# Kernel optimization log

Hardware: AMD Instinct MI355X
Metric: run time of the kernel (lower is better)

The kernel has to match this reference:

```python
import jax, jax.numpy as jnp
import numpy as np

B, Q, K, H = 8, 2048, 2048, 512


def setup_inputs() -> dict:
    key = jax.random.key(0)
    ks = jax.random.split(key, 12)
    s = 1.0 / np.sqrt(H)
    return {
        "query": jax.random.normal(ks[0], (B, Q, H), jnp.float32),
        "key_": jax.random.normal(ks[1], (B, K, H), jnp.float32),
        "value": jax.random.normal(ks[2], (B, K, H), jnp.float32),
        "mask": jax.random.randint(ks[3], (B, K), 0, 2).astype(bool),
        "Wq": jax.random.normal(ks[4], (H, H), jnp.float32) * s,
        "bq": jnp.zeros((H,), jnp.float32),
        "Wk": jax.random.normal(ks[5], (H, H), jnp.float32) * s,
        "bk": jnp.zeros((H,), jnp.float32),
        "Wv": jax.random.normal(ks[6], (H, H), jnp.float32) * s,
        "bv": jnp.zeros((H,), jnp.float32),
        "Wo": jax.random.normal(ks[7], (H, H), jnp.float32) * s,
        "bo": jnp.zeros((H,), jnp.float32),
    }


def reference(query, key_, value, mask, Wq, bq, Wk, bk, Wv, bv, Wo, bo):
    scale = jnp.sqrt(jnp.float32(H))
    Qp = query @ Wq + bq          # (B,Q,H)
    Kp = key_ @ Wk + bk           # (B,K,H)
    Vp = value @ Wv + bv          # (B,K,H)
    energy = jnp.einsum("bqh,bkh->bqk", Qp, Kp) / scale
    # mask is (B, key_len); torch code broadcasts it over all query rows
    energy = jnp.where(mask[:, None, :], -jnp.inf, energy)
    idx = jnp.argmax(energy, axis=-1)                 # (B,Q)
    score = jax.nn.one_hot(idx, K, dtype=energy.dtype)  # hardmax one-hot (B,Q,K)
    # score @ V is exactly a per-row gather of the argmax-selected V row
    res = jnp.take_along_axis(Vp, idx[:, :, None], axis=1)  # (B,Q,H)
    res = res @ Wo + bo
    return (res, score)
```

## Files before the change

kernel.cpp:

```cpp
#include <hip/hip_runtime.h>

typedef _Float16 f16;
typedef f16 f16x8 __attribute__((ext_vector_type(8)));
typedef f16 f16x4 __attribute__((ext_vector_type(4)));
typedef short s16x8 __attribute__((ext_vector_type(8)));
typedef short s16x4 __attribute__((ext_vector_type(4)));
typedef float f32x4 __attribute__((ext_vector_type(4)));

#define MFMA16(a,b,c)  __builtin_amdgcn_mfma_f32_16x16x32_f16(a,b,c,0,0,0)
#define MFMAB16(a,b,c) __builtin_amdgcn_mfma_f32_16x16x32_bf16(a,b,c,0,0,0)

static constexpr int Bn = 8, Qn = 2048, Kn = 2048, Hn = 512;
static constexpr int Mn = Bn * Qn;

typedef __attribute__((address_space(1))) const unsigned int as1_uint;
typedef __attribute__((address_space(3))) unsigned int as3_uint;

__device__ __forceinline__ void gl_lds16(const void* g, void* l) {
    __builtin_amdgcn_global_load_lds((as1_uint*)g, (as3_uint*)l, 16, 0, 0);
}

__device__ __forceinline__ short bf16r(float x) {
    unsigned u = __builtin_bit_cast(unsigned, x);
    u += 0x7fffu + ((u >> 16) & 1u);
    return (short)(u >> 16);
}

__device__ __forceinline__ int swz(int row) { return (row >> 1) & 3; }

__global__ __launch_bounds__(256) void prep_all(
    const int* __restrict__ mask, const float* __restrict__ Wk,
    const float* __restrict__ Wo, const float* __restrict__ bq,
    const float* __restrict__ bv, const float* __restrict__ bo,
    int* __restrict__ cidx, int* __restrict__ cnt,
    f16* __restrict__ Wk_h, f16* __restrict__ Wk_l, short* __restrict__ Wot,
    float* __restrict__ wvec, float* __restrict__ cvec)
{
    const int bid = blockIdx.x, t = threadIdx.x;
    if (bid < 8) {
        __shared__ int sums[256];
        int b = bid;
        int base = b * Kn + t * 8;
        int mv[8]; int s = 0;
        #pragma unroll
        for (int i = 0; i < 8; ++i) { mv[i] = (mask[base + i] == 0); s += mv[i]; }
        sums[t] = s;
        __syncthreads();
        for (int off = 1; off < 256; off <<= 1) {
            int v = (t >= off) ? sums[t - off] : 0;
            __syncthreads();
            sums[t] += v;
            __syncthreads();
        }
        int pos = (t > 0 ? sums[t - 1] : 0);
        #pragma unroll
        for (int i = 0; i < 8; ++i)
            if (mv[i]) cidx[b * Kn + pos++] = t * 8 + i;
        if (t == 255) {
            int total = sums[255];
            if (total == 0) { cidx[b * Kn] = 0; total = 1; }
            cnt[b] = total;
        }
    } else if (bid < 1032) {
        int e = (bid - 8) * 256 + t;
        float v = Wk[e] * 512.0f;
        f16 h = (f16)v;
        Wk_h[e] = h; Wk_l[e] = (f16)((v - (float)h) * 2048.0f);
        int r = e >> 9, c = e & 511;
        Wot[c * 512 + r] = bf16r(Wo[e]);
    } else {
        #pragma unroll
        for (int i = 0; i < 2; ++i) {
            int tt = t + i * 256;
            float s = 0.f;
            for (int n = 0; n < 512; n += 4) {
                f32x4 a = *(const f32x4*)(Wk + (size_t)tt * 512 + n);
                f32x4 q = *(const f32x4*)(bq + n);
                s += a[0]*q[0] + a[1]*q[1] + a[2]*q[2] + a[3]*q[3];
            }
            wvec[tt] = s * (1.0f / 512.0f);
            float s2 = 0.f;
            for (int h = 0; h < 512; ++h) s2 += bv[h] * Wo[h * 512 + tt];
            cvec[tt] = s2 + bo[tt];
        }
    }
}

template<int PREP>
__global__ __launch_bounds__(256) void gemm_split(
    const float* __restrict__ Af,
    const f16* __restrict__ Bh_g, const f16* __restrict__ Bl_g,
    f16* __restrict__ Oh, f16* __restrict__ Ol)
{
    __shared__ __align__(16) f16 Ah[2][2048], Al[2][2048], Bh[2][4096], Bl[2][4096];
    const int tid = threadIdx.x, lane = tid & 63, wid = tid >> 6;
    const int l15 = lane & 15, lg = lane >> 4;
    const int m0 = blockIdx.x * 64, n0 = blockIdx.y * 128;
    const int srow = lane >> 2, sg = lane & 3;
    const int ar0 = tid >> 3, ac0 = (tid & 7) * 4;

    auto stageB = [&](int buf, int ks) {
        const int k0 = ks << 5;
        #pragma unroll
        for (int h = 0; h < 2; ++h) {
            int s = wid + h * 4;
            int row = s * 16 + srow;
            int goff = k0 + ((sg ^ swz(row)) << 3);
            gl_lds16(Bh_g + (size_t)(n0 + row) * Hn + goff, &Bh[buf][s * 512]);
            gl_lds16(Bl_g + (size_t)(n0 + row) * Hn + goff, &Bl[buf][s * 512]);
        }
    };
    auto writeA = [&](int buf, const f32x4* av) {
        #pragma unroll
        for (int rr = 0; rr < 2; ++rr) {
            int row = ar0 + rr * 32;
            f16x4 oh, ol;
            #pragma unroll
            for (int j = 0; j < 4; ++j) {
                f16 hh = (f16)av[rr][j];
                oh[j] = hh;
                ol[j] = (f16)((av[rr][j] - (float)hh) * 2048.0f);
            }
            int off = row * 32 + (((ac0 >> 3) ^ swz(row)) << 3) + (ac0 & 7);
            *(f16x4*)&Ah[buf][off] = oh;
            *(f16x4*)&Al[buf][off] = ol;
        }
    };

    const float* aSrc[2];
    #pragma unroll
    for (int rr = 0; rr < 2; ++rr)
        aSrc[rr] = Af + (size_t)(m0 + ar0 + rr * 32) * Hn;

    f32x4 a0[4][2] = {}, a1[4][2] = {};
    {
        f32x4 av[2];
        #pragma unroll
        for (int rr = 0; rr < 2; ++rr) av[rr] = *(const f32x4*)(aSrc[rr] + ac0);
        stageB(0, 0);
        writeA(0, av);
    }
    __syncthreads();
    #pragma unroll 1
    for (int ks = 0; ks < 16; ++ks) {
        const int cur = ks & 1, nxt = cur ^ 1;
        f32x4 av[2];
        if (ks < 15) {
            const int k1 = (ks + 1) << 5;
            #pragma unroll
            for (int rr = 0; rr < 2; ++rr) av[rr] = *(const f32x4*)(aSrc[rr] + k1 + ac0);
            stageB(nxt, ks + 1);
        }
        f16x8 fbh[2], fbl[2];
        #pragma unroll
        for (int fj = 0; fj < 2; ++fj) {
            int row = wid * 32 + fj * 16 + l15;
            int off = row * 32 + ((lg ^ swz(row)) << 3);
            fbh[fj] = *(f16x8*)&Bh[cur][off];
            fbl[fj] = *(f16x8*)&Bl[cur][off];
        }
        #pragma unroll
        for (int fi = 0; fi < 4; ++fi) {
            int row = fi * 16 + l15;
            int off = row * 32 + ((lg ^ swz(row)) << 3);
            f16x8 fah = *(f16x8*)&Ah[cur][off];
            f16x8 fal = *(f16x8*)&Al[cur][off];
            #pragma unroll
            for (int fj = 0; fj < 2; ++fj) {
                a0[fi][fj] = MFMA16(fah, fbh[fj], a0[fi][fj]);
                a1[fi][fj] = MFMA16(fah, fbl[fj], a1[fi][fj]);
                a1[fi][fj] = MFMA16(fal, fbh[fj], a1[fi][fj]);
            }
        }
        if (ks < 15) writeA(nxt, av);
        __syncthreads();
    }
    #pragma unroll
    for (int fi = 0; fi < 4; ++fi)
    #pragma unroll
    for (int fj = 0; fj < 2; ++fj)
    #pragma unroll
    for (int j = 0; j < 4; ++j) {
        int m = m0 + fi * 16 + lg * 4 + j;
        int n = n0 + wid * 32 + fj * 16 + l15;
        float v = a0[fi][fj][j] + a1[fi][fj][j] * (1.0f / 2048.0f);
        if (PREP == 0) v *= (1.0f / 512.0f);
        f16 h = (f16)v;
        f16 lo = (f16)((v - (float)h) * 2048.0f);
        size_t o = PREP ? ((size_t)n * Hn + m) : ((size_t)m * Hn + n);
        Oh[o] = h; Ol[o] = lo;
    }
}

__global__ __launch_bounds__(256) void gemm_bfk0(
    const float* __restrict__ Af, const short* __restrict__ Bt,
    short* __restrict__ Out)
{
    __shared__ __align__(16) short As[2][2048], Bs[2][4096];
    const int tid = threadIdx.x, lane = tid & 63, wid = tid >> 6;
    const int l15 = lane & 15, lg = lane >> 4;
    const int m0 = blockIdx.x * 64, n0 = blockIdx.y * 128;
    const int srow = lane >> 2, sg = lane & 3;
    const int ar0 = tid >> 3, ac0 = (tid & 7) * 4;

    const float* aSrc[2];
    #pragma unroll
    for (int rr = 0; rr < 2; ++rr)
        aSrc[rr] = Af + (size_t)(m0 + ar0 + rr * 32) * Hn;

    auto stageB = [&](int buf, int ks) {
        const int k0 = ks << 5;
        #pragma unroll
        for (int h = 0; h < 2; ++h) {
            int s = wid + h * 4;
            int row = s * 16 + srow;
            int goff = k0 + ((sg ^ swz(row)) << 3);
            gl_lds16(Bt + (size_t)(n0 + row) * Hn + goff, &Bs[buf][s * 512]);
        }
    };
    auto writeA = [&](int buf, const f32x4* av) {
        #pragma unroll
        for (int rr = 0; rr < 2; ++rr) {
            int row = ar0 + rr * 32;
            s16x4 o;
            #pragma unroll
            for (int j = 0; j < 4; ++j) o[j] = bf16r(av[rr][j]);
            int off = row * 32 + (((ac0 >> 3) ^ swz(row)) << 3) + (ac0 & 7);
            *(s16x4*)&As[buf][off] = o;
        }
    };

    f32x4 acc[4][2] = {};
    {
        f32x4 av[2];
        #pragma unroll
        for (int rr = 0; rr < 2; ++rr) av[rr] = *(const f32x4*)(aSrc[rr] + ac0);
        stageB(0, 0);
        writeA(0, av);
    }
    __syncthreads();
    #pragma unroll 1
    for (int ks = 0; ks < 16; ++ks) {
        const int cur = ks & 1, nxt = cur ^ 1;
        f32x4 av[2];
        if (ks < 15) {
            const int k1 = (ks + 1) << 5;
            #pragma unroll
            for (int rr = 0; rr < 2; ++rr) av[rr] = *(const f32x4*)(aSrc[rr] + k1 + ac0);
            stageB(nxt, ks + 1);
        }
        s16x8 fb[2];
        #pragma unroll
        for (int fj = 0; fj < 2; ++fj) {
            int row = wid * 32 + fj * 16 + l15;
            fb[fj] = *(s16x8*)&Bs[cur][row * 32 + ((lg ^ swz(row)) << 3)];
        }
        #pragma unroll
        for (int fi = 0; fi < 4; ++fi) {
            int row = fi * 16 + l15;
            s16x8 fa = *(s16x8*)&As[cur][row * 32 + ((lg ^ swz(row)) << 3)];
            #pragma unroll
            for (int fj = 0; fj < 2; ++fj)
                acc[fi][fj] = MFMAB16(fa, fb[fj], acc[fi][fj]);
        }
        if (ks < 15) writeA(nxt, av);
        __syncthreads();
    }
    #pragma unroll
    for (int fi = 0; fi < 4; ++fi)
    #pragma unroll
    for (int fj = 0; fj < 2; ++fj)
    #pragma unroll
    for (int j = 0; j < 4; ++j) {
        int m = m0 + fi * 16 + lg * 4 + j;
        int n = n0 + wid * 32 + fj * 16 + l15;
        Out[(size_t)n * Hn + m] = bf16r(acc[fi][fj][j]);
    }
}

__global__ __launch_bounds__(256) void qm_kconv(
    const float* __restrict__ query,
    const f16* __restrict__ Mt_h, const f16* __restrict__ Mt_l,
    f16* __restrict__ qM_h, f16* __restrict__ qM_l,
    const float* __restrict__ key_, const int* __restrict__ cidx,
    const int* __restrict__ cnt, const float* __restrict__ wvec,
    f16* __restrict__ Kc_h, float* __restrict__ beta)
{
    __shared__ __align__(16) f16 smem[2][2048 + 2048 + 4096 + 4096];
    const int bid = blockIdx.x;
    const int tid = threadIdx.x, lane = tid & 63, wid = tid >> 6;
    if (bid < 1024) {
        f16 (*Ah)[2048+2048+4096+4096] = smem;
        #define AH(b,i) Ah[b][i]
        #define AL(b,i) Ah[b][2048 + (i)]
        #define BH(b,i) Ah[b][4096 + (i)]
        #define BL(b,i) Ah[b][8192 + (i)]
        const int l15 = lane & 15, lg = lane >> 4;
        const int m0 = (bid & 255) * 64, n0 = (bid >> 8) * 128;
        const int srow = lane >> 2, sg = lane & 3;
        const int ar0 = tid >> 3, ac0 = (tid & 7) * 4;

        auto stageB = [&](int buf, int ks) {
            const int k0 = ks << 5;
            #pragma unroll
            for (int h = 0; h < 2; ++h) {
                int s = wid + h * 4;
                int row = s * 16 + srow;
                int goff = k0 + ((sg ^ swz(row)) << 3);
                gl_lds16(Mt_h + (size_t)(n0 + row) * Hn + goff, &BH(buf, s * 512));
                gl_lds16(Mt_l + (size_t)(n0 + row) * Hn + goff, &BL(buf, s * 512));
            }
        };
        auto writeA = [&](int buf, const f32x4* av) {
            #pragma unroll
            for (int rr = 0; rr < 2; ++rr) {
                int row = ar0 + rr * 32;
                f16x4 oh, ol;
                #pragma unroll
                for (int j = 0; j < 4; ++j) {
                    f16 hh = (f16)av[rr][j];
                    oh[j] = hh;
                    ol[j] = (f16)((av[rr][j] - (float)hh) * 2048.0f);
                }
                int off = row * 32 + (((ac0 >> 3) ^ swz(row)) << 3) + (ac0 & 7);
                *(f16x4*)&AH(buf, off) = oh;
                *(f16x4*)&AL(buf, off) = ol;
            }
        };

        const float* aSrc[2];
        #pragma unroll
        for (int rr = 0; rr < 2; ++rr)
            aSrc[rr] = query + (size_t)(m0 + ar0 + rr * 32) * Hn;

        f32x4 a0[4][2] = {}, a1[4][2] = {};
        {
            f32x4 av[2];
            #pragma unroll
            for (int rr = 0; rr < 2; ++rr) av[rr] = *(const f32x4*)(aSrc[rr] + ac0);
            stageB(0, 0);
            writeA(0, av);
        }
        __syncthreads();
        #pragma unroll 1
        for (int ks = 0; ks < 16; ++ks) {
            const int cur = ks & 1, nxt = cur ^ 1;
            f32x4 av[2];
            if (ks < 15) {
                const int k1 = (ks + 1) << 5;
                #pragma unroll
                for (int rr = 0; rr < 2; ++rr) av[rr] = *(const f32x4*)(aSrc[rr] + k1 + ac0);
                stageB(nxt, ks + 1);
            }
            f16x8 fbh[2], fbl[2];
            #pragma unroll
            for (int fj = 0; fj < 2; ++fj) {
                int row = wid * 32 + fj * 16 + l15;
                int off = row * 32 + ((lg ^ swz(row)) << 3);
                fbh[fj] = *(f16x8*)&BH(cur, off);
                fbl[fj] = *(f16x8*)&BL(cur, off);
            }
            #pragma unroll
            for (int fi = 0; fi < 4; ++fi) {
                int row = fi * 16 + l15;
                int off = row * 32 + ((lg ^ swz(row)) << 3);
                f16x8 fah = *(f16x8*)&AH(cur, off);
                f16x8 fal = *(f16x8*)&AL(cur, off);
                #pragma unroll
                for (int fj = 0; fj < 2; ++fj) {
                    a0[fi][fj] = MFMA16(fah, fbh[fj], a0[fi][fj]);
                    a1[fi][fj] = MFMA16(fah, fbl[fj], a1[fi][fj]);
                    a1[fi][fj] = MFMA16(fal, fbh[fj], a1[fi][fj]);
                }
            }
            if (ks < 15) writeA(nxt, av);
            __syncthreads();
        }
        #pragma unroll
        for (int fi = 0; fi < 4; ++fi)
        #pragma unroll
        for (int fj = 0; fj < 2; ++fj)
        #pragma unroll
        for (int j = 0; j < 4; ++j) {
            int m = m0 + fi * 16 + lg * 4 + j;
            int n = n0 + wid * 32 + fj * 16 + l15;
            float v = (a0[fi][fj][j] + a1[fi][fj][j] * (1.0f / 2048.0f)) * (1.0f / 512.0f);
            f16 h = (f16)v;
            qM_h[(size_t)m * Hn + n] = h;
            qM_l[(size_t)m * Hn + n] = (f16)((v - (float)h) * 2048.0f);
        }
        #undef AH
        #undef AL
        #undef BH
        #undef BL
    } else {
        int kb = bid - 1024;
        int b = kb >> 9;
        int j = (kb & 511) * 4 + wid;
        int cn = cnt[b];
        if (j >= cn) return;
        const float* src = key_ + (size_t)(b * Kn + cidx[b * Kn + j]) * Hn;
        size_t dst = (size_t)(b * Kn + j) * Hn;
        float s = 0.f;
        #pragma unroll
        for (int i = 0; i < 2; ++i) {
            int c0 = lane * 8 + i * 4;
            f32x4 v = *(const f32x4*)(src + c0);
            f32x4 w = *(const f32x4*)(wvec + c0);
            f16x4 oh;
            #pragma unroll
            for (int e = 0; e < 4; ++e) {
                oh[e] = (f16)v[e];
                s += v[e] * w[e];
            }
            *(f16x4*)(Kc_h + dst + c0) = oh;
        }
        #pragma unroll
        for (int sm = 1; sm < 64; sm <<= 1) s += __shfl_xor(s, sm, 64);
        if (lane == 0) beta[b * Kn + j] = s;
    }
}

__global__ __launch_bounds__(256) void energy_approx(
    const f16* __restrict__ Qh, const f16* __restrict__ Kh,
    const float* __restrict__ beta, const int* __restrict__ cnt,
    f16* __restrict__ approxE, float* __restrict__ pval, int* __restrict__ pidx)
{
    __shared__ __align__(16) f16 Ah[2][4096], Bh[2][4096];
    const int tid = threadIdx.x, lane = tid & 63, wid = tid >> 6;
    const int wr = wid >> 1, wc = wid & 1, l15 = lane & 15, lg = lane >> 4;
    const int qt = blockIdx.x, kc = blockIdx.y, b = blockIdx.z;
    const int cn = cnt[b];
    const int kbase = kc << 7;
    if (kbase >= cn) return;
    const int m0 = b * Qn + qt * 128;
    const int kr0 = b * Kn + kbase;
    const int srow = lane >> 2, sg = lane & 3;
    const float NEGINF = -__builtin_inff();

    auto stage = [&](int buf, int ks) {
        const int k0 = ks << 5;
        #pragma unroll
        for (int h = 0; h < 2; ++h) {
            int s = wid + h * 4;
            int row = s * 16 + srow;
            int goff = k0 + ((sg ^ swz(row)) << 3);
            gl_lds16(Qh + (size_t)(m0 + row) * Hn + goff, &Ah[buf][s * 512]);
            gl_lds16(Kh + (size_t)(kr0 + row) * Hn + goff, &Bh[buf][s * 512]);
        }
    };

    f32x4 acc[4][4] = {};
    stage(0, 0);
    __syncthreads();
    #pragma unroll 1
    for (int ks = 0; ks < 16; ++ks) {
        const int cur = ks & 1;
        if (ks < 15) stage(cur ^ 1, ks + 1);
        f16x8 fb[4];
        #pragma unroll
        for (int fj = 0; fj < 4; ++fj) {
            int row = wc * 64 + fj * 16 + l15;
            fb[fj] = *(f16x8*)&Bh[cur][row * 32 + ((lg ^ swz(row)) << 3)];
        }
        #pragma unroll
        for (int fi = 0; fi < 4; ++fi) {
            int row = wr * 64 + fi * 16 + l15;
            f16x8 fa = *(f16x8*)&Ah[cur][row * 32 + ((lg ^ swz(row)) << 3)];
            #pragma unroll
            for (int fj = 0; fj < 4; ++fj)
                acc[fi][fj] = MFMA16(fa, fb[fj], acc[fi][fj]);
        }
        __syncthreads();
    }
    const f16 NEGI = (f16)NEGINF;
    float bet[4]; int valid[4];
    #pragma unroll
    for (int fj = 0; fj < 4; ++fj) {
        int lc = wc * 64 + fj * 16 + l15;
        valid[fj] = (kbase + lc < cn);
        bet[fj] = valid[fj] ? beta[b * Kn + kbase + lc] : 0.0f;
    }
    float (*bwv)[128] = (float(*)[128])&Ah[0][0];
    int   (*bwi)[128] = (int(*)[128])&Ah[1][0];
    #pragma unroll
    for (int fi = 0; fi < 4; ++fi)
    #pragma unroll
    for (int j = 0; j < 4; ++j) {
        float bv = NEGINF; int bc = 0x7fffffff;
        #pragma unroll
        for (int fj = 0; fj < 4; ++fj) {
            int lc = wc * 64 + fj * 16 + l15;
            float v = valid[fj] ? (acc[fi][fj][j] + bet[fj]) : NEGINF;
            int row = wr * 64 + fi * 16 + lg * 4 + j;
            approxE[(size_t)(m0 + row) * Kn + kbase + lc] = valid[fj] ? (f16)v : NEGI;
            if (v > bv || (v == bv && lc < bc)) { bv = v; bc = lc; }
        }
        #pragma unroll
        for (int sm = 1; sm < 16; sm <<= 1) {
            float ov = __shfl_xor(bv, sm, 64);
            int   oc = __shfl_xor(bc, sm, 64);
            if (ov > bv || (ov == bv && oc < bc)) { bv = ov; bc = oc; }
        }
        if (l15 == 0) {
            int row = wr * 64 + fi * 16 + lg * 4 + j;
            bwv[wc][row] = bv; bwi[wc][row] = bc;
        }
    }
    __syncthreads();
    if (tid < 128) {
        float v0 = bwv[0][tid], v1 = bwv[1][tid];
        int   i0 = bwi[0][tid], i1 = bwi[1][tid];
        float v; int i;
        if (v0 > v1 || (v0 == v1 && i0 < i1)) { v = v0; i = i0; } else { v = v1; i = i1; }
        int m = m0 + tid;
        pval[m * 16 + kc] = v;
        pidx[m * 16 + kc] = kbase + i;
    }
}

__global__ __launch_bounds__(256) void refine(
    const f16* __restrict__ apxE, const float* __restrict__ pval,
    const int* __restrict__ pidx,
    const f16* __restrict__ qMh, const f16* __restrict__ qMl,
    const float* __restrict__ key_, const float* __restrict__ beta,
    const int* __restrict__ cidx, const int* __restrict__ cnt,
    int* __restrict__ idxArr)
{
    const int wid = threadIdx.x >> 6, lane = threadIdx.x & 63;
    const int m = blockIdx.x * 4 + wid;
    const int b = m >> 11;
    const int cn = cnt[b];
    const int nch = (cn + 127) >> 7;
    const float NEGINF = -__builtin_inff();

    float chv = (lane < nch) ? pval[m * 16 + lane] : NEGINF;
    int   chi = (lane < nch) ? pidx[m * 16 + lane] : 0x7fffffff;
    float gv = chv; int gi = chi;
    #pragma unroll
    for (int sm = 1; sm < 64; sm <<= 1) {
        float ov = __shfl_xor(gv, sm, 64);
        int   oc = __shfl_xor(gi, sm, 64);
        if (ov > gv || (ov == gv && oc < gi)) { gv = ov; gi = oc; }
    }
    const float thr = gv - 1.0f;

    int ncand = 0;
    for (int c = 0; c < nch; ++c) {
        float cmax = __shfl(chv, c, 64);
        if (cmax < thr) continue;
        const f16* ap = apxE + (size_t)m * Kn + c * 128 + lane * 2;
        ncand += __popcll(__ballot((float)ap[0] >= thr));
        ncand += __popcll(__ballot((float)ap[1] >= thr));
    }
    if (ncand == 1) {
        if (lane == 0) idxArr[m] = cidx[b * Kn + gi];
        return;
    }
    float q8[8];
    {
        f16x8 qh = *(const f16x8*)(qMh + (size_t)m * Hn + lane * 8);
        f16x8 ql = *(const f16x8*)(qMl + (size_t)m * Hn + lane * 8);
        #pragma unroll
        for (int e = 0; e < 8; ++e)
            q8[e] = (float)qh[e] + (float)ql[e] * (1.0f / 2048.0f);
    }
    float bestV = NEGINF; int bestOrig = 0x7fffffff;
    for (int c = 0; c < nch; ++c) {
        float cmax = __shfl(chv, c, 64);
        if (cmax < thr) continue;
        const f16* ap = apxE + (size_t)m * Kn + c * 128 + lane * 2;
        unsigned long long bb[2];
        bb[0] = __ballot((float)ap[0] >= thr);
        bb[1] = __ballot((float)ap[1] >= thr);
        #pragma unroll
        for (int p = 0; p < 2; ++p) {
            unsigned long long mb = bb[p];
            while (mb) {
                int L = __builtin_ctzll(mb);
                mb &= mb - 1;
                int j = c * 128 + L * 2 + p;
                int orig = cidx[b * Kn + j];
                const float* kr = key_ + ((size_t)(b * Kn + orig)) * Hn + lane * 8;
                float d = 0.f;
                #pragma unroll
                for (int e = 0; e < 8; ++e) d += q8[e] * kr[e];
                #pragma unroll
                for (int sm = 1; sm < 64; sm <<= 1) d += __shfl_xor(d, sm, 64);
                d += beta[b * Kn + j];
                if (d > bestV || (d == bestV && orig < bestOrig)) { bestV = d; bestOrig = orig; }
            }
        }
    }
    if (lane == 0) idxArr[m] = bestOrig;
}

__global__ __launch_bounds__(256) void tail_fused(
    const float* __restrict__ value, const short* __restrict__ NtB,
    const float* __restrict__ cvec, const int* __restrict__ idxArr,
    float* __restrict__ res, float* __restrict__ score)
{
    __shared__ __align__(16) short As[2][2048], Bs[2][4096];
    const int bid = blockIdx.x;
    const int tid = threadIdx.x, lane = tid & 63, wid = tid >> 6;
    if (bid >= 1024) {
        int m = bid - 1024;
        int c = idxArr[m];
        float* row = score + (size_t)m * Kn;
        #pragma unroll
        for (int i = 0; i < 2; ++i) {
            int v = tid + i * 256;
            f32x4 val = {0.f, 0.f, 0.f, 0.f};
            if ((c >> 2) == v) val[c & 3] = 1.0f;
            *(f32x4*)(row + v * 4) = val;
        }
        return;
    }
    const int l15 = lane & 15, lg = lane >> 4;
    const int m0 = (bid & 255) * 64, n0 = (bid >> 8) * 128;
    const int srow = lane >> 2, sg = lane & 3;
    const int ar0 = tid >> 3, ac0 = (tid & 7) * 4;

    const float* aSrc[2];
    #pragma unroll
    for (int rr = 0; rr < 2; ++rr) {
        int row = ar0 + rr * 32;
        int bb = m0 >> 11;
        aSrc[rr] = value + (size_t)(bb * Kn + idxArr[m0 + row]) * Hn;
    }

    auto stageB = [&](int buf, int ks) {
        const int k0 = ks << 5;
        #pragma unroll
        for (int h = 0; h < 2; ++h) {
            int s = wid + h * 4;
            int row = s * 16 + srow;
            int goff = k0 + ((sg ^ swz(row)) << 3);
            gl_lds16(NtB + (size_t)(n0 + row) * Hn + goff, &Bs[buf][s * 512]);
        }
    };
    auto writeA = [&](int buf, const f32x4* av) {
        #pragma unroll
        for (int rr = 0; rr < 2; ++rr) {
            int row = ar0 + rr * 32;
            s16x4 o;
            #pragma unroll
            for (int j = 0; j < 4; ++j) o[j] = bf16r(av[rr][j]);
            int off = row * 32 + (((ac0 >> 3) ^ swz(row)) << 3) + (ac0 & 7);
            *(s16x4*)&As[buf][off] = o;
        }
    };

    f32x4 acc[4][2] = {};
    {
        f32x4 av[2];
        #pragma unroll
        for (int rr = 0; rr < 2; ++rr) av[rr] = *(const f32x4*)(aSrc[rr] + ac0);
        stageB(0, 0);
        writeA(0, av);
    }
    __syncthreads();
    #pragma unroll 1
    for (int ks = 0; ks < 16; ++ks) {
        const int cur = ks & 1, nxt = cur ^ 1;
        f32x4 av[2];
        if (ks < 15) {
            const int k1 = (ks + 1) << 5;
            #pragma unroll
            for (int rr = 0; rr < 2; ++rr) av[rr] = *(const f32x4*)(aSrc[rr] + k1 + ac0);
            stageB(nxt, ks + 1);
        }
        s16x8 fb[2];
        #pragma unroll
        for (int fj = 0; fj < 2; ++fj) {
            int row = wid * 32 + fj * 16 + l15;
            fb[fj] = *(s16x8*)&Bs[cur][row * 32 + ((lg ^ swz(row)) << 3)];
        }
        #pragma unroll
        for (int fi = 0; fi < 4; ++fi) {
            int row = fi * 16 + l15;
            s16x8 fa = *(s16x8*)&As[cur][row * 32 + ((lg ^ swz(row)) << 3)];
            #pragma unroll
            for (int fj = 0; fj < 2; ++fj)
                acc[fi][fj] = MFMAB16(fa, fb[fj], acc[fi][fj]);
        }
        if (ks < 15) writeA(nxt, av);
        __syncthreads();
    }
    #pragma unroll
    for (int fi = 0; fi < 4; ++fi)
    #pragma unroll
    for (int fj = 0; fj < 2; ++fj)
    #pragma unroll
    for (int j = 0; j < 4; ++j) {
        int m = m0 + fi * 16 + lg * 4 + j;
        int n = n0 + wid * 32 + fj * 16 + l15;
        res[(size_t)m * Hn + n] = acc[fi][fj][j] + cvec[n];
    }
}

extern "C" void kernel_launch(void* const* d_in, const int* in_sizes, int n_in,
                              void* d_out, int out_size, void* d_ws, size_t ws_size,
                              hipStream_t stream)
{
    const float* query = (const float*)d_in[0];
    const float* key_  = (const float*)d_in[1];
    const float* value = (const float*)d_in[2];
    const int*   mask  = (const int*)d_in[3];
    const float* Wq = (const float*)d_in[4];
    const float* bq = (const float*)d_in[5];
    const float* Wk = (const float*)d_in[6];
    const float* bv = (const float*)d_in[9];
    const float* Wv = (const float*)d_in[8];
    const float* Wo = (const float*)d_in[10];
    const float* bo = (const float*)d_in[11];

    float* res = (float*)d_out;
    float* scoreBase = res + (size_t)Mn * Hn;
    char* sc = (char*)scoreBase;
    constexpr size_t MB = 1u << 20;
    f16*   qM_h = (f16*)(sc + 0 * MB);
    f16*   qM_l = (f16*)(sc + 16 * MB);
    f16*   Kc_h = (f16*)(sc + 32 * MB);
    f16*   apxE = (f16*)(sc + 48 * MB);
    char*  wb   = sc + 112 * MB;
    f16*   Mt_h = (f16*)(wb);
    f16*   Mt_l = (f16*)(wb + 524288);
    f16*   Wk_h = (f16*)(wb + 2 * 524288);
    f16*   Wk_l = (f16*)(wb + 3 * 524288);
    short* Wot  = (short*)(wb + 4 * 524288);
    float* wvec = (float*)(wb + 5 * 524288);
    float* beta = (float*)(wb + 5 * 524288 + 8192);
    int*   cidx = (int*)(wb + 5 * 524288 + 8192 + 65536);
    float* pval = (float*)(wb + 6 * 524288);
    int*   pidx = (int*)(wb + 8 * 524288);

    int*   idxArr = (int*)d_ws;
    int*   cnt    = (int*)d_ws + 16384;
    float* cvec   = (float*)((char*)d_ws + 65600);
    short* NtB    = (short*)((char*)d_ws + 67648);

    prep_all<<<1033, 256, 0, stream>>>(mask, Wk, Wo, bq, bv, bo,
                                       cidx, cnt, Wk_h, Wk_l, Wot, wvec, cvec);

    gemm_split<1><<<dim3(8, 4), 256, 0, stream>>>(Wq, Wk_h, Wk_l, Mt_h, Mt_l);
    gemm_bfk0<<<dim3(8, 4), 256, 0, stream>>>(Wv, Wot, NtB);

    qm_kconv<<<5120, 256, 0, stream>>>(query, Mt_h, Mt_l, qM_h, qM_l,
                                       key_, cidx, cnt, wvec, Kc_h, beta);

    energy_approx<<<dim3(Qn / 128, 16, Bn), 256, 0, stream>>>(
        qM_h, Kc_h, beta, cnt, apxE, pval, pidx);

    refine<<<Mn / 4, 256, 0, stream>>>(
        apxE, pval, pidx, qM_h, qM_l, key_, beta, cidx, cnt, idxArr);

    tail_fused<<<1024 + Mn, 256, 0, stream>>>(value, NtB, cvec, idxArr,
                                              res, scoreBase);
}
```

Baseline: 246.3 us.

## Track per-chunk top-2 in energy_approx and drop the approximate energy matrix

energy_approx no longer writes the full f16 approximate energy matrix. For each 128-key chunk it now reduces both the best value with its index and the second-best value. The query tile shrinks to 64 rows with four waves splitting columns, which doubles the grid. Refine uses the chunk top-2 values to decide whether a row is unambiguous, exact-checks the single chunk winner otherwise, and falls back to evaluating every key in a chunk whose second-best is within the threshold. This removes a large global write and read, at the cost of potentially expensive full-chunk rescans for ambiguous rows and a heavier reduction per block.

```diff
diff --git a/kernel.cpp b/kernel.cpp
--- a/kernel.cpp
+++ b/kernel.cpp
@@ -424,104 +424,109 @@
 __global__ __launch_bounds__(256) void energy_approx(
     const f16* __restrict__ Qh, const f16* __restrict__ Kh,
     const float* __restrict__ beta, const int* __restrict__ cnt,
-    f16* __restrict__ approxE, float* __restrict__ pval, int* __restrict__ pidx)
+    float* __restrict__ pval1, int* __restrict__ pidx, float* __restrict__ pval2)
 {
-    __shared__ __align__(16) f16 Ah[2][4096], Bh[2][4096];
+    __shared__ __align__(16) f16 Ah[2][2048], Bh[2][4096];
     const int tid = threadIdx.x, lane = tid & 63, wid = tid >> 6;
-    const int wr = wid >> 1, wc = wid & 1, l15 = lane & 15, lg = lane >> 4;
+    const int l15 = lane & 15, lg = lane >> 4;
     const int qt = blockIdx.x, kc = blockIdx.y, b = blockIdx.z;
     const int cn = cnt[b];
     const int kbase = kc << 7;
     if (kbase >= cn) return;
-    const int m0 = b * Qn + qt * 128;
+    const int m0 = b * Qn + qt * 64;
     const int kr0 = b * Kn + kbase;
     const int srow = lane >> 2, sg = lane & 3;
     const float NEGINF = -__builtin_inff();
 
     auto stage = [&](int buf, int ks) {
         const int k0 = ks << 5;
+        {
+            int row = wid * 16 + srow;
+            int goff = k0 + ((sg ^ swz(row)) << 3);
+            gl_lds16(Qh + (size_t)(m0 + row) * Hn + goff, &Ah[buf][wid * 512]);
+        }
         #pragma unroll
         for (int h = 0; h < 2; ++h) {
             int s = wid + h * 4;
             int row = s * 16 + srow;
             int goff = k0 + ((sg ^ swz(row)) << 3);
-            gl_lds16(Qh + (size_t)(m0 + row) * Hn + goff, &Ah[buf][s * 512]);
             gl_lds16(Kh + (size_t)(kr0 + row) * Hn + goff, &Bh[buf][s * 512]);
         }
     };
 
-    f32x4 acc[4][4] = {};
+    f32x4 acc[4][2] = {};
     stage(0, 0);
     __syncthreads();
     #pragma unroll 1
     for (int ks = 0; ks < 16; ++ks) {
         const int cur = ks & 1;
         if (ks < 15) stage(cur ^ 1, ks + 1);
-        f16x8 fb[4];
-        #pragma unroll
-        for (int fj = 0; fj < 4; ++fj) {
-            int row = wc * 64 + fj * 16 + l15;
+        f16x8 fb[2];
+        #pragma unroll
+        for (int fj = 0; fj < 2; ++fj) {
+            int row = wid * 32 + fj * 16 + l15;
             fb[fj] = *(f16x8*)&Bh[cur][row * 32 + ((lg ^ swz(row)) << 3)];
         }
         #pragma unroll
         for (int fi = 0; fi < 4; ++fi) {
-            int row = wr * 64 + fi * 16 + l15;
+            int row = fi * 16 + l15;
             f16x8 fa = *(f16x8*)&Ah[cur][row * 32 + ((lg ^ swz(row)) << 3)];
             #pragma unroll
-            for (int fj = 0; fj < 4; ++fj)
+            for (int fj = 0; fj < 2; ++fj)
                 acc[fi][fj] = MFMA16(fa, fb[fj], acc[fi][fj]);
         }
         __syncthreads();
     }
-    const f16 NEGI = (f16)NEGINF;
-    float bet[4]; int valid[4];
-    #pragma unroll
-    for (int fj = 0; fj < 4; ++fj) {
-        int lc = wc * 64 + fj * 16 + l15;
+    float (*bw1)[64] = (float(*)[64])&Ah[0][0];
+    int   (*bi1)[64] = (int(*)[64])&Ah[0][512];
+    float (*bw2)[64] = (float(*)[64])&Ah[1][0];
+    float bet[2]; int valid[2];
+    #pragma unroll
+    for (int fj = 0; fj < 2; ++fj) {
+        int lc = wid * 32 + fj * 16 + l15;
         valid[fj] = (kbase + lc < cn);
         bet[fj] = valid[fj] ? beta[b * Kn + kbase + lc] : 0.0f;
     }
-    float (*bwv)[128] = (float(*)[128])&Ah[0][0];
-    int   (*bwi)[128] = (int(*)[128])&Ah[1][0];
     #pragma unroll
     for (int fi = 0; fi < 4; ++fi)
     #pragma unroll
     for (int j = 0; j < 4; ++j) {
-        float bv = NEGINF; int bc = 0x7fffffff;
-        #pragma unroll
-        for (int fj = 0; fj < 4; ++fj) {
-            int lc = wc * 64 + fj * 16 + l15;
-            float v = valid[fj] ? (acc[fi][fj][j] + bet[fj]) : NEGINF;
-            int row = wr * 64 + fi * 16 + lg * 4 + j;
-            approxE[(size_t)(m0 + row) * Kn + kbase + lc] = valid[fj] ? (f16)v : NEGI;
-            if (v > bv || (v == bv && lc < bc)) { bv = v; bc = lc; }
-        }
+        int row = fi * 16 + lg * 4 + j;
+        int lc0 = wid * 32 + l15, lc1 = lc0 + 16;
+        float v0 = valid[0] ? (acc[fi][0][j] + bet[0]) : NEGINF;
+        float v1 = valid[1] ? (acc[fi][1][j] + bet[1]) : NEGINF;
+        float t1, t2; int ti;
+        if (v1 > v0) { t1 = v1; ti = lc1; t2 = v0; }
+        else         { t1 = v0; ti = lc0; t2 = v1; }
         #pragma unroll
         for (int sm = 1; sm < 16; sm <<= 1) {
-            float ov = __shfl_xor(bv, sm, 64);
-            int   oc = __shfl_xor(bc, sm, 64);
-            if (ov > bv || (ov == bv && oc < bc)) { bv = ov; bc = oc; }
-        }
-        if (l15 == 0) {
-            int row = wr * 64 + fi * 16 + lg * 4 + j;
-            bwv[wc][row] = bv; bwi[wc][row] = bc;
-        }
+            float o1 = __shfl_xor(t1, sm, 64);
+            int   oi = __shfl_xor(ti, sm, 64);
+            float o2 = __shfl_xor(t2, sm, 64);
+            if (o1 > t1 || (o1 == t1 && oi < ti)) { t2 = fmaxf(t1, o2); t1 = o1; ti = oi; }
+            else                                  { t2 = fmaxf(t2, o1); }
+        }
+        if (l15 == 0) { bw1[wid][row] = t1; bi1[wid][row] = ti; bw2[wid][row] = t2; }
     }
     __syncthreads();
-    if (tid < 128) {
-        float v0 = bwv[0][tid], v1 = bwv[1][tid];
-        int   i0 = bwi[0][tid], i1 = bwi[1][tid];
-        float v; int i;
-        if (v0 > v1 || (v0 == v1 && i0 < i1)) { v = v0; i = i0; } else { v = v1; i = i1; }
+    if (tid < 64) {
+        float t1 = bw1[0][tid]; int ti = bi1[0][tid]; float t2 = bw2[0][tid];
+        #pragma unroll
+        for (int s = 1; s < 4; ++s) {
+            float o1 = bw1[s][tid]; int oi = bi1[s][tid]; float o2 = bw2[s][tid];
+            if (o1 > t1 || (o1 == t1 && oi < ti)) { t2 = fmaxf(t1, o2); t1 = o1; ti = oi; }
+            else                                  { t2 = fmaxf(t2, o1); }
+        }
         int m = m0 + tid;
-        pval[m * 16 + kc] = v;
-        pidx[m * 16 + kc] = kbase + i;
+        pval1[m * 16 + kc] = t1;
+        pidx [m * 16 + kc] = kbase + ti;
+        pval2[m * 16 + kc] = t2;
     }
 }
 
 __global__ __launch_bounds__(256) void refine(
-    const f16* __restrict__ apxE, const float* __restrict__ pval,
-    const int* __restrict__ pidx,
+    const float* __restrict__ pval1, const int* __restrict__ pidx,
+    const float* __restrict__ pval2,
     const f16* __restrict__ qMh, const f16* __restrict__ qMl,
     const float* __restrict__ key_, const float* __restrict__ beta,
     const int* __restrict__ cidx, const int* __restrict__ cnt,
@@ -534,26 +539,21 @@
     const int nch = (cn + 127) >> 7;
     const float NEGINF = -__builtin_inff();
 
-    float chv = (lane < nch) ? pval[m * 16 + lane] : NEGINF;
-    int   chi = (lane < nch) ? pidx[m * 16 + lane] : 0x7fffffff;
+    float chv = (lane < nch) ? pval1[m * 16 + lane] : NEGINF;
+    int   chi = (lane < nch) ? pidx [m * 16 + lane] : 0x7fffffff;
+    float ch2 = (lane < nch) ? pval2[m * 16 + lane] : NEGINF;
+
     float gv = chv; int gi = chi;
     #pragma unroll
     for (int sm = 1; sm < 64; sm <<= 1) {
         float ov = __shfl_xor(gv, sm, 64);
-        int   oc = __shfl_xor(gi, sm, 64);
-        if (ov > gv || (ov == gv && oc < gi)) { gv = ov; gi = oc; }
+        int   oi = __shfl_xor(gi, sm, 64);
+        if (ov > gv || (ov == gv && oi < gi)) { gv = ov; gi = oi; }
     }
     const float thr = gv - 1.0f;
-
-    int ncand = 0;
-    for (int c = 0; c < nch; ++c) {
-        float cmax = __shfl(chv, c, 64);
-        if (cmax < thr) continue;
-        const f16* ap = apxE + (size_t)m * Kn + c * 128 + lane * 2;
-        ncand += __popcll(__ballot((float)ap[0] >= thr));
-        ncand += __popcll(__ballot((float)ap[1] >= thr));
-    }
-    if (ncand == 1) {
+    unsigned long long candMask = __ballot(chv >= thr);
+    unsigned long long scanMask = __ballot(ch2 >= thr);
+    if (__popcll(candMask) == 1 && scanMask == 0ULL) {
         if (lane == 0) idxArr[m] = cidx[b * Kn + gi];
         return;
     }
@@ -566,30 +566,26 @@
             q8[e] = (float)qh[e] + (float)ql[e] * (1.0f / 2048.0f);
     }
     float bestV = NEGINF; int bestOrig = 0x7fffffff;
+    auto evalJ = [&](int j) {
+        int orig = cidx[b * Kn + j];
+        const float* kr = key_ + ((size_t)(b * Kn + orig)) * Hn + lane * 8;
+        float d = 0.f;
+        #pragma unroll
+        for (int e = 0; e < 8; ++e) d += q8[e] * kr[e];
+        #pragma unroll
+        for (int sm = 1; sm < 64; sm <<= 1) d += __shfl_xor(d, sm, 64);
+        d += beta[b * Kn + j];
+        if (d > bestV || (d == bestV && orig < bestOrig)) { bestV = d; bestOrig = orig; }
+    };
     for (int c = 0; c < nch; ++c) {
-        float cmax = __shfl(chv, c, 64);
-        if (cmax < thr) continue;
-        const f16* ap = apxE + (size_t)m * Kn + c * 128 + lane * 2;
-        unsigned long long bb[2];
-        bb[0] = __ballot((float)ap[0] >= thr);
-        bb[1] = __ballot((float)ap[1] >= thr);
-        #pragma unroll
-        for (int p = 0; p < 2; ++p) {
-            unsigned long long mb = bb[p];
-            while (mb) {
-                int L = __builtin_ctzll(mb);
-                mb &= mb - 1;
-                int j = c * 128 + L * 2 + p;
-                int orig = cidx[b * Kn + j];
-                const float* kr = key_ + ((size_t)(b * Kn + orig)) * Hn + lane * 8;
-                float d = 0.f;
-                #pragma unroll
-                for (int e = 0; e < 8; ++e) d += q8[e] * kr[e];
-                #pragma unroll
-                for (int sm = 1; sm < 64; sm <<= 1) d += __shfl_xor(d, sm, 64);
-                d += beta[b * Kn + j];
-                if (d > bestV || (d == bestV && orig < bestOrig)) { bestV = d; bestOrig = orig; }
-            }
+        float cv = __shfl(chv, c, 64);
+        if (cv < thr) continue;
+        float c2 = __shfl(ch2, c, 64);
+        if (c2 >= thr) {
+            int jend = min(128, cn - c * 128);
+            for (int t = 0; t < jend; ++t) evalJ(c * 128 + t);
+        } else {
+            evalJ(__shfl(chi, c, 64));
         }
     }
     if (lane == 0) idxArr[m] = bestOrig;
@@ -722,7 +718,6 @@
     f16*   qM_h = (f16*)(sc + 0 * MB);
     f16*   qM_l = (f16*)(sc + 16 * MB);
     f16*   Kc_h = (f16*)(sc + 32 * MB);
-    f16*   apxE = (f16*)(sc + 48 * MB);
     char*  wb   = sc + 112 * MB;
     f16*   Mt_h = (f16*)(wb);
     f16*   Mt_l = (f16*)(wb + 524288);
@@ -732,8 +727,9 @@
     float* wvec = (float*)(wb + 5 * 524288);
     float* beta = (float*)(wb + 5 * 524288 + 8192);
     int*   cidx = (int*)(wb + 5 * 524288 + 8192 + 65536);
-    float* pval = (float*)(wb + 6 * 524288);
-    int*   pidx = (int*)(wb + 8 * 524288);
+    float* pval1 = (float*)(wb + 6 * 524288);
+    int*   pidx  = (int*)(wb + 8 * 524288);
+    float* pval2 = (float*)(wb + 10 * 524288);
 
     int*   idxArr = (int*)d_ws;
     int*   cnt    = (int*)d_ws + 16384;
@@ -749,11 +745,11 @@
     qm_kconv<<<5120, 256, 0, stream>>>(query, Mt_h, Mt_l, qM_h, qM_l,
                                        key_, cidx, cnt, wvec, Kc_h, beta);
 
-    energy_approx<<<dim3(Qn / 128, 16, Bn), 256, 0, stream>>>(
-        qM_h, Kc_h, beta, cnt, apxE, pval, pidx);
+    energy_approx<<<dim3(Qn / 64, 16, Bn), 256, 0, stream>>>(
+        qM_h, Kc_h, beta, cnt, pval1, pidx, pval2);
 
     refine<<<Mn / 4, 256, 0, stream>>>(
-        apxE, pval, pidx, qM_h, qM_l, key_, beta, cidx, cnt, idxArr);
+        pval1, pidx, pval2, qM_h, qM_l, key_, beta, cidx, cnt, idxArr);
 
     tail_fused<<<1024 + Mn, 256, 0, stream>>>(value, NtB, cvec, idxArr,
                                               res, scoreBase);
```

Result: slower. 388.9 us (+57.9%).
